# Optimization experiments

Measured on AMD Instinct MI355X. Metric: run time of the kernel, lower is better.

The kernel has to match this reference:

```python
import jax, jax.numpy as jnp
import numpy as np

B, S, I, H = 256, 50, 1024, 512
SENT, DOC = 512, 1024
SEGMENTS, MAXPOS = 4, 25
POS_SZ, SEG_SZ = 50, 50


def _gru_dir(xg, W_hh, b_hh):
    # xg: [S,B,3H] precomputed input gates; returns hidden states [S,B,H]
    Hh = W_hh.shape[1]

    def step(h, xg_t):
        hg = h @ W_hh.T + b_hh  # [B,3H]
        r = jax.nn.sigmoid(xg_t[:, :Hh] + hg[:, :Hh])
        z = jax.nn.sigmoid(xg_t[:, Hh:2 * Hh] + hg[:, Hh:2 * Hh])
        n = jnp.tanh(xg_t[:, 2 * Hh:] + r * hg[:, 2 * Hh:])
        h = (1.0 - z) * n + z * h
        return h, h

    h0 = jnp.zeros((xg.shape[1], Hh), xg.dtype)
    _, hs = jax.lax.scan(step, h0, xg)
    return hs


def setup_inputs() -> dict:
    key = jax.random.key(0)
    ks = jax.random.split(key, 24)
    sc = 0.05
    inp = {
        'x': jax.random.normal(ks[0], (B, S, I), jnp.float32),
        'num_sentences': jnp.full((B,), S, jnp.int32),
        # GRU forward direction
        'W_ih_f': jax.random.normal(ks[1], (3 * H, I), jnp.float32) * sc,
        'W_hh_f': jax.random.normal(ks[2], (3 * H, H), jnp.float32) * sc,
        'b_ih_f': jax.random.normal(ks[3], (3 * H,), jnp.float32) * sc,
        'b_hh_f': jax.random.normal(ks[4], (3 * H,), jnp.float32) * sc,
        # GRU backward direction
        'W_ih_b': jax.random.normal(ks[5], (3 * H, I), jnp.float32) * sc,
        'W_hh_b': jax.random.normal(ks[6], (3 * H, H), jnp.float32) * sc,
        'b_ih_b': jax.random.normal(ks[7], (3 * H,), jnp.float32) * sc,
        'b_hh_b': jax.random.normal(ks[8], (3 * H,), jnp.float32) * sc,
        # sentence_rep: Linear(2H -> SENT) + ReLU
        'W_sent': jax.random.normal(ks[9], (SENT, 2 * H), jnp.float32) * sc,
        'b_sent': jax.random.normal(ks[10], (SENT,), jnp.float32) * sc,
        # content_logits: Linear(SENT -> 1)
        'w_content': jax.random.normal(ks[11], (SENT,), jnp.float32) * sc,
        'b_content': jax.random.normal(ks[12], (1,), jnp.float32) * sc,
        # document_rep: Linear(SENT->DOC), tanh, Linear(DOC->SENT)
        'W_d1': jax.random.normal(ks[13], (DOC, SENT), jnp.float32) * sc,
        'b_d1': jax.random.normal(ks[14], (DOC,), jnp.float32) * sc,
        'W_d2': jax.random.normal(ks[15], (SENT, DOC), jnp.float32) * sc,
        'b_d2': jax.random.normal(ks[16], (SENT,), jnp.float32) * sc,
        # Bilinear(SENT, SENT, 1, bias=False) weight
        'W_sim': jax.random.normal(ks[17], (SENT, SENT), jnp.float32) * sc,
        'bias': jnp.zeros((1,), jnp.float32),
        # position / segment encoders (embedding row 0 is padding -> zeros)
        'pos_emb': (jax.random.normal(ks[18], (MAXPOS + 1, POS_SZ), jnp.float32) * sc).at[0].set(0.0),
        'pos_lin': jax.random.normal(ks[19], (POS_SZ,), jnp.float32) * sc,
        'seg_emb': (jax.random.normal(ks[20], (SEGMENTS + 1, SEG_SZ), jnp.float32) * sc).at[0].set(0.0),
        'seg_lin': jax.random.normal(ks[21], (SEG_SZ,), jnp.float32) * sc,
    }
    return inp


def reference(x, num_sentences, W_ih_f, W_hh_f, b_ih_f, b_hh_f,
              W_ih_b, W_hh_b, b_ih_b, b_hh_b,
              W_sent, b_sent, w_content, b_content,
              W_d1, b_d1, W_d2, b_d2, W_sim, bias,
              pos_emb, pos_lin, seg_emb, seg_lin):
    xs = jnp.transpose(x, (1, 0, 2))  # [S,B,I] (time-major, uniform lengths)

    # Bidirectional GRU
    xg_f = jnp.einsum('sbi,gi->sbg', xs, W_ih_f) + b_ih_f
    hs_f = _gru_dir(xg_f, W_hh_f, b_hh_f)  # [S,B,H]
    xg_b = jnp.einsum('sbi,gi->sbg', xs[::-1], W_ih_b) + b_ih_b
    hs_b = _gru_dir(xg_b, W_hh_b, b_hh_b)[::-1]  # [S,B,H]
    rnn_out = jnp.concatenate([hs_f, hs_b], axis=-1)  # [S,B,2H]
    rnn_out = jnp.transpose(rnn_out, (1, 0, 2))  # [B,S,2H]

    # sentence representations
    sent = jax.nn.relu(jnp.einsum('bsh,dh->bsd', rnn_out, W_sent) + b_sent)  # [B,S,SENT]

    content = jnp.einsum('bsd,d->bs', sent, w_content) + b_content[0]

    avg = sent.sum(axis=1) / num_sentences[:, None].astype(sent.dtype)  # [B,SENT]
    doc = jnp.tanh(avg @ W_d1.T + b_d1) @ W_d2.T + b_d2  # [B,SENT]
    salience = jnp.einsum('bsd,bd->bs', sent, doc)

    # position / segment logits (faithful to original ordering: rel computed pre-clamp)
    abs_pos = jnp.arange(1, S + 1)[None, :].astype(jnp.float32)  # [1,S]
    chunk = jnp.round(num_sentences.astype(jnp.float32) / SEGMENTS)[:, None]  # [B,1]
    rel = jnp.clip(jnp.ceil(abs_pos / chunk), 0, SEGMENTS).astype(jnp.int32)  # [B,S]
    abs_idx = jnp.clip(jnp.arange(1, S + 1), 0, MAXPOS)  # [S]
    pos_logits = pos_emb[abs_idx] @ pos_lin  # [S]
    seg_logits = seg_emb[rel] @ seg_lin  # [B,S]

    static = content + salience + pos_logits[None, :] + seg_logits + bias[0]  # [B,S]

    # sequential novelty scan
    def step(summary, inputs):
        s_t, static_t = inputs  # [B,SENT], [B]
        sim = jnp.einsum('bi,ij,bj->b', s_t, W_sim, jnp.tanh(summary))
        logit = static_t - sim
        summary = summary + s_t * jax.nn.sigmoid(logit)[:, None]
        return summary, logit

    sent_tm = jnp.transpose(sent, (1, 0, 2))  # [S,B,SENT]
    summary0 = jnp.zeros((x.shape[0], SENT), sent.dtype)
    _, logits = jax.lax.scan(step, summary0, (sent_tm, static.T))  # [S,B]
    return logits[:, :, None]  # [S,B,1]
```

## Files before the change

kernel.cpp:

```cpp
#include <hip/hip_runtime.h>
#include <hip/hip_bf16.h>
#include <math.h>

#define B_    256
#define S_    50
#define I_    1024
#define H_    512
#define G3_   1536
#define SENT_ 512
#define DOC_  1024

typedef short bf16x8 __attribute__((ext_vector_type(8)));
typedef float f32x4 __attribute__((ext_vector_type(4)));

__device__ __forceinline__ float sigf(float x) { return 1.0f / (1.0f + __expf(-x)); }

__device__ __forceinline__ void gload16(const void* g, void* l) {
  __builtin_amdgcn_global_load_lds((const __attribute__((address_space(1))) void*)g,
                                   (__attribute__((address_space(3))) void*)l, 16, 0, 0);
}

__global__ __launch_bounds__(256) void mfma_xg(
    const __hip_bfloat16* __restrict__ x,
    const __hip_bfloat16* __restrict__ Wf, const float* __restrict__ bf_,
    const __hip_bfloat16* __restrict__ Wb, const float* __restrict__ bb_,
    __hip_bfloat16* __restrict__ xgf, __hip_bfloat16* __restrict__ xgb) {
  __shared__ __align__(16) short As[128 * 64];
  __shared__ __align__(16) short Ws[128 * 64];
  const int dir = blockIdx.z;
  const __hip_bfloat16* W = dir ? Wb : Wf;
  const float* bias = dir ? bb_ : bf_;
  __hip_bfloat16* out = dir ? xgb : xgf;
  const int tid = threadIdx.x;
  const int m0 = blockIdx.y * 128, n0 = blockIdx.x * 128;
  const int s = blockIdx.y >> 1, b_base = (blockIdx.y & 1) * 128;
  const int s_eff = dir ? (S_ - 1 - s) : s;
  const int lane = tid & 63, w = tid >> 6;
  const int moff = (w & 1) * 64, noff = (w >> 1) * 64;
  const int frow = lane & 15, quad = lane >> 4;
  const int rr = tid >> 3, gs = tid & 7;
  f32x4 acc[4][4] = {};
  for (int kc = 0; kc < I_; kc += 64) {
#pragma unroll
    for (int iss = 0; iss < 4; iss++) {
      int r = iss * 32 + rr;
      int col = kc + ((gs ^ (r & 7)) << 3);
      gload16(x + ((size_t)(b_base + r) * S_ + s_eff) * I_ + col, &As[(iss * 256 + w * 64) * 8]);
    }
#pragma unroll
    for (int iss = 0; iss < 4; iss++) {
      int r = iss * 32 + rr;
      int col = kc + ((gs ^ (r & 7)) << 3);
      gload16(W + (size_t)(n0 + r) * I_ + col, &Ws[(iss * 256 + w * 64) * 8]);
    }
    __syncthreads();
#pragma unroll
    for (int ks = 0; ks < 2; ks++) {
      int kg = ks * 4 + quad;
      bf16x8 af[4], bfr[4];
#pragma unroll
      for (int mf = 0; mf < 4; mf++) {
        int r = moff + mf * 16 + frow;
        af[mf] = *(const bf16x8*)&As[(r * 8 + (kg ^ (r & 7))) * 8];
      }
#pragma unroll
      for (int nf = 0; nf < 4; nf++) {
        int r = noff + nf * 16 + frow;
        bfr[nf] = *(const bf16x8*)&Ws[(r * 8 + (kg ^ (r & 7))) * 8];
      }
#pragma unroll
      for (int mf = 0; mf < 4; mf++)
#pragma unroll
        for (int nf = 0; nf < 4; nf++)
          acc[mf][nf] = __builtin_amdgcn_mfma_f32_16x16x32_bf16(af[mf], bfr[nf], acc[mf][nf], 0, 0, 0);
    }
    __syncthreads();
  }
#pragma unroll
  for (int mf = 0; mf < 4; mf++) {
    int rowb = m0 + moff + mf * 16 + quad * 4;
#pragma unroll
    for (int nf = 0; nf < 4; nf++) {
      int col = n0 + noff + nf * 16 + frow;
      float bv = bias[col];
      f32x4 c = acc[mf][nf];
#pragma unroll
      for (int rg = 0; rg < 4; rg++)
        out[(size_t)(rowb + rg) * G3_ + col] = __float2bfloat16(c[rg] + bv);
    }
  }
}

template <int ACT, bool HASBIAS>
__global__ __launch_bounds__(256) void mfma_nt(
    const __hip_bfloat16* __restrict__ A, const __hip_bfloat16* __restrict__ W,
    const float* __restrict__ bias, __hip_bfloat16* __restrict__ outb, int N, int K) {
  __shared__ __align__(16) short As[128 * 64];
  __shared__ __align__(16) short Ws[128 * 64];
  const int tid = threadIdx.x;
  const int m0 = blockIdx.y * 128, n0 = blockIdx.x * 128;
  const int lane = tid & 63, w = tid >> 6;
  const int moff = (w & 1) * 64, noff = (w >> 1) * 64;
  const int frow = lane & 15, quad = lane >> 4;
  const int rr = tid >> 3, gs = tid & 7;
  f32x4 acc[4][4] = {};
  for (int kc = 0; kc < K; kc += 64) {
#pragma unroll
    for (int iss = 0; iss < 4; iss++) {
      int r = iss * 32 + rr;
      int col = kc + ((gs ^ (r & 7)) << 3);
      gload16(A + (size_t)(m0 + r) * K + col, &As[(iss * 256 + w * 64) * 8]);
    }
#pragma unroll
    for (int iss = 0; iss < 4; iss++) {
      int r = iss * 32 + rr;
      int col = kc + ((gs ^ (r & 7)) << 3);
      gload16(W + (size_t)(n0 + r) * K + col, &Ws[(iss * 256 + w * 64) * 8]);
    }
    __syncthreads();
#pragma unroll
    for (int ks = 0; ks < 2; ks++) {
      int kg = ks * 4 + quad;
      bf16x8 af[4], bfr[4];
#pragma unroll
      for (int mf = 0; mf < 4; mf++) {
        int r = moff + mf * 16 + frow;
        af[mf] = *(const bf16x8*)&As[(r * 8 + (kg ^ (r & 7))) * 8];
      }
#pragma unroll
      for (int nf = 0; nf < 4; nf++) {
        int r = noff + nf * 16 + frow;
        bfr[nf] = *(const bf16x8*)&Ws[(r * 8 + (kg ^ (r & 7))) * 8];
      }
#pragma unroll
      for (int mf = 0; mf < 4; mf++)
#pragma unroll
        for (int nf = 0; nf < 4; nf++)
          acc[mf][nf] = __builtin_amdgcn_mfma_f32_16x16x32_bf16(af[mf], bfr[nf], acc[mf][nf], 0, 0, 0);
    }
    __syncthreads();
  }
#pragma unroll
  for (int mf = 0; mf < 4; mf++) {
    int rowb = m0 + moff + mf * 16 + quad * 4;
#pragma unroll
    for (int nf = 0; nf < 4; nf++) {
      int col = n0 + noff + nf * 16 + frow;
      float bv = HASBIAS ? bias[col] : 0.f;
      f32x4 c = acc[mf][nf];
#pragma unroll
      for (int rg = 0; rg < 4; rg++) {
        float v = c[rg] + bv;
        if (ACT == 1) v = fmaxf(v, 0.f);
        outb[(size_t)(rowb + rg) * N + col] = __float2bfloat16(v);
      }
    }
  }
}

__global__ __launch_bounds__(256, 1) void gru_persistent(
    const __hip_bfloat16* __restrict__ xgf, const __hip_bfloat16* __restrict__ xgb,
    const __hip_bfloat16* __restrict__ Wpf, const __hip_bfloat16* __restrict__ Wpb,
    const float* __restrict__ bhhf, const float* __restrict__ bhhb,
    __hip_bfloat16* __restrict__ h16a, __hip_bfloat16* __restrict__ h16b,
    __hip_bfloat16* __restrict__ rnn,
    unsigned int* __restrict__ arrive) {
  __shared__ __align__(16) short Hs[32 * 512];
  const int bid = blockIdx.x;
  const int dir = bid >> 7;
  const int bt = (bid >> 4) & 7;
  const int jt = bid & 15;
  const int gi = bid >> 4;
  const int tid = threadIdx.x;
  const int w = tid >> 6, lane = tid & 63;
  const int frow = lane & 15, quad = lane >> 4;
  const int wm = w & 1, wn = w >> 1;
  const __hip_bfloat16* xg = dir ? xgb : xgf;
  const __hip_bfloat16* Wp = dir ? Wpb : Wpf;
  const float* bhh = dir ? bhhb : bhhf;

  unsigned int* my_flag = arrive + (size_t)bid * 64;

  const int j = jt * 32 + wn * 16 + frow;
  const int brow0 = bt * 32 + wm * 16 + quad * 4;
  const int ar = wm * 16 + frow;
  const float br = bhh[j], bz = bhh[H_ + j], bn = bhh[2 * H_ + j];

  bf16x8 wf[3][16];
#pragma unroll
  for (int g = 0; g < 3; g++)
#pragma unroll
    for (int ks = 0; ks < 16; ks++)
      wf[g][ks] = *(const bf16x8*)(Wp + (size_t)((jt * 2 + wn) * 48 + g * 16 + frow) * H_ +
                                   ks * 32 + quad * 8);

  float hreg[4] = {0.f, 0.f, 0.f, 0.f};
  union U16 { unsigned long long q[2]; bf16x8 v; };

  for (int t = 0; t < S_; t++) {
    const __hip_bfloat16* hp = (t & 1) ? h16b : h16a;
    __hip_bfloat16* hn = (t & 1) ? h16a : h16b;
    float xgv[4][3];
#pragma unroll
    for (int rg = 0; rg < 4; rg++) {
      const __hip_bfloat16* xr = xg + ((size_t)t * B_ + brow0 + rg) * G3_;
      xgv[rg][0] = __bfloat162float(xr[j]);
      xgv[rg][1] = __bfloat162float(xr[H_ + j]);
      xgv[rg][2] = __bfloat162float(xr[2 * H_ + j]);
    }
    const __hip_bfloat16* hbase = hp + (size_t)(dir * B_ + bt * 32) * H_;
#pragma unroll
    for (int i = 0; i < 8; i++) {
      int c = i * 256 + tid;
      int r = c >> 6, kg = c & 63;
      const unsigned long long* p = (const unsigned long long*)(hbase + (size_t)r * H_ + kg * 8);
      U16 u;
      u.q[0] = __hip_atomic_load(p, __ATOMIC_RELAXED, __HIP_MEMORY_SCOPE_AGENT);
      u.q[1] = __hip_atomic_load(p + 1, __ATOMIC_RELAXED, __HIP_MEMORY_SCOPE_AGENT);
      int q = r * 64 + (kg & 56) + ((kg & 7) ^ (r & 7));
      *(bf16x8*)&Hs[q * 8] = u.v;
    }
    __syncthreads();
    bf16x8 af[16];
#pragma unroll
    for (int ks = 0; ks < 16; ks++) {
      int g2 = ks * 4 + quad;
      int q = ar * 64 + (g2 & 56) + ((g2 & 7) ^ (ar & 7));
      af[ks] = *(const bf16x8*)&Hs[q * 8];
    }
    f32x4 acc[3] = {};
#pragma unroll
    for (int ks = 0; ks < 16; ks++)
#pragma unroll
      for (int g = 0; g < 3; g++)
        acc[g] = __builtin_amdgcn_mfma_f32_16x16x32_bf16(af[ks], wf[g][ks], acc[g], 0, 0, 0);

    const int s_orig = dir ? (S_ - 1 - t) : t;
#pragma unroll
    for (int rg = 0; rg < 4; rg++) {
      int b = brow0 + rg;
      float r = sigf(xgv[rg][0] + acc[0][rg] + br);
      float z = sigf(xgv[rg][1] + acc[1][rg] + bz);
      float n = tanhf(xgv[rg][2] + r * (acc[2][rg] + bn));
      float h = (1.f - z) * n + z * hreg[rg];
      hreg[rg] = h;
      __hip_bfloat16 hb = __float2bfloat16(h);
      unsigned short us;
      __builtin_memcpy(&us, &hb, 2);
      __hip_atomic_store((unsigned short*)(hn + (size_t)(dir * B_ + b) * H_ + j), us,
                         __ATOMIC_RELAXED, __HIP_MEMORY_SCOPE_AGENT);
      rnn[((size_t)b * S_ + s_orig) * (2 * H_) + dir * H_ + j] = hb;
    }

    if (t + 1 < S_) {
      __syncthreads();
      if (tid == 0)
        __hip_atomic_store(my_flag, (unsigned)(t + 1), __ATOMIC_RELAXED,
                           __HIP_MEMORY_SCOPE_AGENT);
      if (w == 0) {
        unsigned int* fl = arrive + (size_t)(gi * 16 + (lane & 15)) * 64;
        for (int spin = 0; spin < (1 << 17); spin++) {
          unsigned v = (lane < 16)
                           ? __hip_atomic_load(fl, __ATOMIC_RELAXED, __HIP_MEMORY_SCOPE_AGENT)
                           : (unsigned)(t + 1);
          if (__ballot(v >= (unsigned)(t + 1)) == ~0ull) break;
          __builtin_amdgcn_s_sleep(1);
        }
      }
      __syncthreads();
    }
  }
}

template <int ACT>
__global__ __launch_bounds__(256) void gemm_nt(const float* __restrict__ A,
                                               const float* __restrict__ W,
                                               const float* __restrict__ bias,
                                               float* __restrict__ C, int N, int K) {
  __shared__ float As[16][68];
  __shared__ float Bs[16][68];
  const int t = threadIdx.x;
  const int tx = t & 15, ty = t >> 4;
  const int m0 = blockIdx.y * 64, n0 = blockIdx.x * 64;
  const int lr = t >> 2, lc = t & 3;
  const float* Arow = A + (size_t)(m0 + lr) * K;
  const float* Wrow = W + (size_t)(n0 + lr) * K;
  float acc[4][4] = {};
  for (int kc = 0; kc < K; kc += 16) {
    float4 av = *(const float4*)(Arow + kc + lc * 4);
    float4 wv = *(const float4*)(Wrow + kc + lc * 4);
    As[lc * 4 + 0][lr] = av.x; As[lc * 4 + 1][lr] = av.y;
    As[lc * 4 + 2][lr] = av.z; As[lc * 4 + 3][lr] = av.w;
    Bs[lc * 4 + 0][lr] = wv.x; Bs[lc * 4 + 1][lr] = wv.y;
    Bs[lc * 4 + 2][lr] = wv.z; Bs[lc * 4 + 3][lr] = wv.w;
    __syncthreads();
#pragma unroll
    for (int k = 0; k < 16; k++) {
      float4 a4 = *(const float4*)&As[k][ty * 4];
      float4 b4 = *(const float4*)&Bs[k][tx * 4];
      float ar[4] = {a4.x, a4.y, a4.z, a4.w};
      float br[4] = {b4.x, b4.y, b4.z, b4.w};
#pragma unroll
      for (int i = 0; i < 4; i++)
#pragma unroll
        for (int jx = 0; jx < 4; jx++) acc[i][jx] = fmaf(ar[i], br[jx], acc[i][jx]);
    }
    __syncthreads();
  }
  float4 bv = *(const float4*)&bias[n0 + tx * 4];
  float bb[4] = {bv.x, bv.y, bv.z, bv.w};
#pragma unroll
  for (int i = 0; i < 4; i++) {
    float o[4];
#pragma unroll
    for (int jx = 0; jx < 4; jx++) {
      float v = acc[i][jx] + bb[jx];
      if (ACT == 1) v = fmaxf(v, 0.f);
      if (ACT == 2) v = tanhf(v);
      o[jx] = v;
    }
    *(float4*)&C[(size_t)(m0 + ty * 4 + i) * N + n0 + tx * 4] = float4{o[0], o[1], o[2], o[3]};
  }
}

#define PREP_CAST1   1536
#define PREP_CAST2   3072
#define PREP_CAST3   3584
#define PREP_PACK1   4352
#define PREP_PACK2   5120
#define PREP_TSIM    6144
#define PREP_ZH      6272
#define PREP_ZF      6288
#define PREP_POS     6289
__global__ __launch_bounds__(256) void prep_all(
    const float* __restrict__ Wihf, const float* __restrict__ Wihb,
    const float* __restrict__ Wsent, const float* __restrict__ Whhf,
    const float* __restrict__ Whhb, const float* __restrict__ Wsim,
    const float* __restrict__ pos_emb, const float* __restrict__ pos_lin,
    const float* __restrict__ seg_emb, const float* __restrict__ seg_lin,
    __hip_bfloat16* __restrict__ Wihf_b, __hip_bfloat16* __restrict__ Wihb_b,
    __hip_bfloat16* __restrict__ Wsent_b, __hip_bfloat16* __restrict__ Wpf,
    __hip_bfloat16* __restrict__ Wpb, __hip_bfloat16* __restrict__ WsimT_b,
    __hip_bfloat16* __restrict__ h16a, unsigned int* __restrict__ arrive,
    float* __restrict__ pos_logits, float* __restrict__ seg_vals) {
  const int blk = blockIdx.x, tid = threadIdx.x;
  if (blk < PREP_CAST2) {
    const float* src = (blk < PREP_CAST1) ? Wihf : Wihb;
    __hip_bfloat16* dst = (blk < PREP_CAST1) ? Wihf_b : Wihb_b;
    int lb = (blk < PREP_CAST1) ? blk : blk - PREP_CAST1;
    int i = lb * 1024 + tid * 4;
    float4 v = *(const float4*)(src + i);
    dst[i] = __float2bfloat16(v.x); dst[i + 1] = __float2bfloat16(v.y);
    dst[i + 2] = __float2bfloat16(v.z); dst[i + 3] = __float2bfloat16(v.w);
  } else if (blk < PREP_CAST3) {
    int i = (blk - PREP_CAST2) * 1024 + tid * 4;
    float4 v = *(const float4*)(Wsent + i);
    Wsent_b[i] = __float2bfloat16(v.x); Wsent_b[i + 1] = __float2bfloat16(v.y);
    Wsent_b[i + 2] = __float2bfloat16(v.z); Wsent_b[i + 3] = __float2bfloat16(v.w);
  } else if (blk < PREP_PACK2) {
    const float* src = (blk < PREP_PACK1) ? Whhf : Whhb;
    __hip_bfloat16* dst = (blk < PREP_PACK1) ? Wpf : Wpb;
    int lb = (blk < PREP_PACK1) ? blk - PREP_CAST3 : blk - PREP_PACK1;
    int e = lb * 1024 + tid * 4;
    int row = e >> 9, k = e & 511;
    int g = row >> 9, j = row & 511;
    int p = (j >> 4) * 48 + g * 16 + (j & 15);
    float4 v = *(const float4*)(src + (size_t)row * 512 + k);
    __hip_bfloat16* d = dst + (size_t)p * 512 + k;
    d[0] = __float2bfloat16(v.x); d[1] = __float2bfloat16(v.y);
    d[2] = __float2bfloat16(v.z); d[3] = __float2bfloat16(v.w);
  } else if (blk < PREP_TSIM) {
    int idx = (blk - PREP_PACK2) * 256 + tid;
    int i = idx >> 9, j = idx & 511;
    WsimT_b[(size_t)j * 512 + i] = __float2bfloat16(Wsim[idx]);
  } else if (blk < PREP_ZH) {
    int i = (blk - PREP_TSIM) * 2048 + tid * 8;
    float4 z = {0.f, 0.f, 0.f, 0.f};
    *(float4*)((short*)h16a + i) = z;
  } else if (blk < PREP_ZF) {
    int i = (blk - PREP_ZH) * 1024 + tid * 4;
    float4 z = {0.f, 0.f, 0.f, 0.f};
    *(float4*)(arrive + i) = z;
  } else {
    if (tid < S_) {
      int idx = tid + 1; if (idx > 25) idx = 25;
      float a = 0.f;
      for (int k = 0; k < 50; k++) a += pos_emb[idx * 50 + k] * pos_lin[k];
      pos_logits[tid] = a;
    }
    if (tid < 5) {
      float a = 0.f;
      for (int k = 0; k < 50; k++) a += seg_emb[tid * 50 + k] * seg_lin[k];
      seg_vals[tid] = a;
    }
  }
}

__global__ void cast_kernel(const float* __restrict__ in, __hip_bfloat16* __restrict__ out, int n) {
  int i = (blockIdx.x * blockDim.x + threadIdx.x) * 4;
  if (i + 3 < n) {
    float4 v = *(const float4*)(in + i);
    out[i + 0] = __float2bfloat16(v.x);
    out[i + 1] = __float2bfloat16(v.y);
    out[i + 2] = __float2bfloat16(v.z);
    out[i + 3] = __float2bfloat16(v.w);
  }
}

__global__ __launch_bounds__(256) void avg_kernel(const __hip_bfloat16* __restrict__ sent,
                                                  const int* __restrict__ ns,
                                                  float* __restrict__ avg) {
  int b = blockIdx.x, tid = threadIdx.x;
  const __hip_bfloat16* base = sent + (size_t)b * S_ * SENT_;
  float a0 = 0.f, a1 = 0.f;
  for (int s = 0; s < S_; s++) {
    a0 += __bfloat162float(base[s * SENT_ + tid]);
    a1 += __bfloat162float(base[s * SENT_ + 256 + tid]);
  }
  float inv = 1.0f / (float)ns[b];
  avg[(size_t)b * SENT_ + tid] = a0 * inv;
  avg[(size_t)b * SENT_ + 256 + tid] = a1 * inv;
}

__global__ __launch_bounds__(64) void static_kernel(
    const __hip_bfloat16* __restrict__ sent, const float* __restrict__ doc,
    const float* __restrict__ wcont, const float* __restrict__ bcont,
    const int* __restrict__ ns, const float* __restrict__ pos_logits,
    const float* __restrict__ seg_vals, const float* __restrict__ bias,
    float* __restrict__ st) {
  int bs = blockIdx.x;
  int b = bs / S_, s = bs % S_;
  int lane = threadIdx.x;
  const __hip_bfloat16* sr = sent + (size_t)bs * SENT_;
  const float* dr = doc + (size_t)b * SENT_;
  float a0 = 0.f, a1 = 0.f;
#pragma unroll
  for (int ii = 0; ii < 8; ii++) {
    int k = ii * 64 + lane;
    float v = __bfloat162float(sr[k]);
    a0 += v * wcont[k];
    a1 += v * dr[k];
  }
#pragma unroll
  for (int off = 32; off; off >>= 1) {
    a0 += __shfl_down(a0, off);
    a1 += __shfl_down(a1, off);
  }
  if (lane == 0) {
    float chunk = rintf((float)ns[b] * 0.25f);
    float relf = ceilf((float)(s + 1) / chunk);
    relf = fminf(fmaxf(relf, 0.f), 4.f);
    int rel = (int)relf;
    st[s * B_ + b] = a0 + bcont[0] + a1 + pos_logits[s] + seg_vals[rel] + bias[0];
  }
}

__global__ __launch_bounds__(256) void novelty_all(
    const __hip_bfloat16* __restrict__ sent, const __hip_bfloat16* __restrict__ U,
    const float* __restrict__ st, float* __restrict__ out) {
  __shared__ float wred[4];
  int b = blockIdx.x, tid = threadIdx.x;
  float s0 = 0.f, s1 = 0.f;
  for (int t = 0; t < S_; t++) {
    const __hip_bfloat16* ur = U + ((size_t)b * S_ + t) * SENT_;
    float p = __bfloat162float(ur[tid]) * tanhf(s0) +
              __bfloat162float(ur[tid + 256]) * tanhf(s1);
#pragma unroll
    for (int off = 32; off; off >>= 1) p += __shfl_down(p, off);
    if ((tid & 63) == 0) wred[tid >> 6] = p;
    __syncthreads();
    float sim = wred[0] + wred[1] + wred[2] + wred[3];
    float logit = st[t * B_ + b] - sim;
    if (tid == 0) out[(size_t)t * B_ + b] = logit;
    float sg = sigf(logit);
    const __hip_bfloat16* sr = sent + ((size_t)b * S_ + t) * SENT_;
    s0 += __bfloat162float(sr[tid]) * sg;
    s1 += __bfloat162float(sr[tid + 256]) * sg;
    __syncthreads();
  }
}

extern "C" void kernel_launch(void* const* d_in, const int* in_sizes, int n_in,
                              void* d_out, int out_size, void* d_ws, size_t ws_size,
                              hipStream_t stream) {
  const float* x = (const float*)d_in[0];
  const int* ns = (const int*)d_in[1];
  const float* Wihf = (const float*)d_in[2];
  const float* Whhf = (const float*)d_in[3];
  const float* bihf = (const float*)d_in[4];
  const float* bhhf = (const float*)d_in[5];
  const float* Wihb = (const float*)d_in[6];
  const float* Whhb = (const float*)d_in[7];
  const float* bihb = (const float*)d_in[8];
  const float* bhhb = (const float*)d_in[9];
  const float* Wsent = (const float*)d_in[10];
  const float* bsent = (const float*)d_in[11];
  const float* wcont = (const float*)d_in[12];
  const float* bcont = (const float*)d_in[13];
  const float* Wd1 = (const float*)d_in[14];
  const float* bd1 = (const float*)d_in[15];
  const float* Wd2 = (const float*)d_in[16];
  const float* bd2 = (const float*)d_in[17];
  const float* Wsim = (const float*)d_in[18];
  const float* bias = (const float*)d_in[19];
  const float* pos_emb = (const float*)d_in[20];
  const float* pos_lin = (const float*)d_in[21];
  const float* seg_emb = (const float*)d_in[22];
  const float* seg_lin = (const float*)d_in[23];
  float* out = (float*)d_out;

  char* base = (char*)d_ws;
  size_t off = 0;
  auto alloc = [&](size_t bytes) { char* p = base + off; off += (bytes + 255) & ~255ull; return p; };
  __hip_bfloat16* xgf_b  = (__hip_bfloat16*)alloc((size_t)S_ * B_ * G3_ * 2);
  __hip_bfloat16* xgb_b  = (__hip_bfloat16*)alloc((size_t)S_ * B_ * G3_ * 2);
  char* region1          = alloc((size_t)B_ * S_ * I_ * 2);
  __hip_bfloat16* x_bf   = (__hip_bfloat16*)region1;
  __hip_bfloat16* sent_b = (__hip_bfloat16*)region1;
  __hip_bfloat16* U_b    = (__hip_bfloat16*)(region1 + (size_t)B_ * S_ * SENT_ * 2);
  __hip_bfloat16* rnn_b  = (__hip_bfloat16*)alloc((size_t)B_ * S_ * 2 * H_ * 2);
  __hip_bfloat16* Wihf_b = (__hip_bfloat16*)alloc((size_t)G3_ * I_ * 2);
  __hip_bfloat16* Wihb_b = (__hip_bfloat16*)alloc((size_t)G3_ * I_ * 2);
  __hip_bfloat16* Wpf    = (__hip_bfloat16*)alloc((size_t)G3_ * H_ * 2);
  __hip_bfloat16* Wpb    = (__hip_bfloat16*)alloc((size_t)G3_ * H_ * 2);
  __hip_bfloat16* Wsent_b= (__hip_bfloat16*)alloc((size_t)SENT_ * 2 * H_ * 2);
  __hip_bfloat16* WsimT_b= (__hip_bfloat16*)alloc((size_t)SENT_ * SENT_ * 2);
  __hip_bfloat16* h16a   = (__hip_bfloat16*)alloc(2 * (size_t)B_ * H_ * 2);
  __hip_bfloat16* h16b   = (__hip_bfloat16*)alloc(2 * (size_t)B_ * H_ * 2);
  unsigned int* arrive   = (unsigned int*)alloc(256 * 64 * 4);
  float* avg             = (float*)alloc((size_t)B_ * SENT_ * 4);
  float* d1buf           = (float*)alloc((size_t)B_ * DOC_ * 4);
  float* doc             = (float*)alloc((size_t)B_ * SENT_ * 4);
  float* st              = (float*)alloc((size_t)S_ * B_ * 4);
  float* poslog          = (float*)alloc(256);
  float* segvals         = (float*)alloc(64);
  (void)ws_size;

  prep_all<<<PREP_POS + 1, 256, 0, stream>>>(
      Wihf, Wihb, Wsent, Whhf, Whhb, Wsim, pos_emb, pos_lin, seg_emb, seg_lin,
      Wihf_b, Wihb_b, Wsent_b, Wpf, Wpb, WsimT_b, h16a, arrive, poslog, segvals);
  cast_kernel<<<(B_ * S_ * I_ / 4 + 255) / 256, 256, 0, stream>>>(x, x_bf, B_ * S_ * I_);

  mfma_xg<<<dim3(G3_ / 128, (S_ * B_) / 128, 2), 256, 0, stream>>>(x_bf, Wihf_b, bihf, Wihb_b, bihb, xgf_b, xgb_b);

  gru_persistent<<<dim3(256), dim3(256), 0, stream>>>(
      xgf_b, xgb_b, Wpf, Wpb, bhhf, bhhb, h16a, h16b, rnn_b, arrive);

  mfma_nt<1, true><<<dim3(SENT_ / 128, (B_ * S_) / 128), 256, 0, stream>>>(rnn_b, Wsent_b, bsent, sent_b, SENT_, 2 * H_);
  avg_kernel<<<B_, 256, 0, stream>>>(sent_b, ns, avg);
  gemm_nt<2><<<dim3(DOC_ / 64, B_ / 64), 256, 0, stream>>>(avg, Wd1, bd1, d1buf, DOC_, SENT_);
  gemm_nt<0><<<dim3(SENT_ / 64, B_ / 64), 256, 0, stream>>>(d1buf, Wd2, bd2, doc, SENT_, DOC_);
  static_kernel<<<B_ * S_, 64, 0, stream>>>(sent_b, doc, wcont, bcont, ns, poslog, segvals, bias, st);

  mfma_nt<0, false><<<dim3(SENT_ / 128, (B_ * S_) / 128), 256, 0, stream>>>(sent_b, WsimT_b, nullptr, U_b, SENT_, SENT_);

  novelty_all<<<B_, 256, 0, stream>>>(sent_b, U_b, st, out);
}
```

Baseline: 695.5 us.

## Fuse x cast into prep, prefetch GRU gates, and shrink novelty/static kernels

Folds the x fp32-to-bf16 cast into the prep kernel to drop one launch. Prefetches the next timestep's input gates before the GRU inter-block barrier so the load latency overlaps the wait. Tiles the Wsim transpose through shared memory for coalesced access, packs four static-logit rows per 256-thread block, and replaces the 256-thread novelty scan with a single-wavefront version using vectorised loads and no block barriers. The costs are more register pressure in the persistent GRU kernel and less parallelism per batch row in the novelty scan.

```diff
diff --git a/kernel.cpp b/kernel.cpp
--- a/kernel.cpp
+++ b/kernel.cpp
@@ -14,6 +14,12 @@
 typedef float f32x4 __attribute__((ext_vector_type(4)));
 
 __device__ __forceinline__ float sigf(float x) { return 1.0f / (1.0f + __expf(-x)); }
+__device__ __forceinline__ float b2f(short s) {
+  unsigned u = ((unsigned)(unsigned short)s) << 16;
+  float f;
+  __builtin_memcpy(&f, &u, 4);
+  return f;
+}
 
 __device__ __forceinline__ void gload16(const void* g, void* l) {
   __builtin_amdgcn_global_load_lds((const __attribute__((address_space(1))) void*)g,
@@ -197,17 +203,18 @@
   float hreg[4] = {0.f, 0.f, 0.f, 0.f};
   union U16 { unsigned long long q[2]; bf16x8 v; };
 
+  float xgv[4][3];
+#pragma unroll
+  for (int rg = 0; rg < 4; rg++) {
+    const __hip_bfloat16* xr = xg + ((size_t)(brow0 + rg)) * G3_;
+    xgv[rg][0] = __bfloat162float(xr[j]);
+    xgv[rg][1] = __bfloat162float(xr[H_ + j]);
+    xgv[rg][2] = __bfloat162float(xr[2 * H_ + j]);
+  }
+
   for (int t = 0; t < S_; t++) {
     const __hip_bfloat16* hp = (t & 1) ? h16b : h16a;
     __hip_bfloat16* hn = (t & 1) ? h16a : h16b;
-    float xgv[4][3];
-#pragma unroll
-    for (int rg = 0; rg < 4; rg++) {
-      const __hip_bfloat16* xr = xg + ((size_t)t * B_ + brow0 + rg) * G3_;
-      xgv[rg][0] = __bfloat162float(xr[j]);
-      xgv[rg][1] = __bfloat162float(xr[H_ + j]);
-      xgv[rg][2] = __bfloat162float(xr[2 * H_ + j]);
-    }
     const __hip_bfloat16* hbase = hp + (size_t)(dir * B_ + bt * 32) * H_;
 #pragma unroll
     for (int i = 0; i < 8; i++) {
@@ -253,6 +260,14 @@
     }
 
     if (t + 1 < S_) {
+      float xgn[4][3];
+#pragma unroll
+      for (int rg = 0; rg < 4; rg++) {
+        const __hip_bfloat16* xr = xg + ((size_t)(t + 1) * B_ + brow0 + rg) * G3_;
+        xgn[rg][0] = __bfloat162float(xr[j]);
+        xgn[rg][1] = __bfloat162float(xr[H_ + j]);
+        xgn[rg][2] = __bfloat162float(xr[2 * H_ + j]);
+      }
       __syncthreads();
       if (tid == 0)
         __hip_atomic_store(my_flag, (unsigned)(t + 1), __ATOMIC_RELAXED,
@@ -268,6 +283,10 @@
         }
       }
       __syncthreads();
+#pragma unroll
+      for (int rg = 0; rg < 4; rg++) {
+        xgv[rg][0] = xgn[rg][0]; xgv[rg][1] = xgn[rg][1]; xgv[rg][2] = xgn[rg][2];
+      }
     }
   }
 }
@@ -323,31 +342,39 @@
   }
 }
 
-#define PREP_CAST1   1536
-#define PREP_CAST2   3072
-#define PREP_CAST3   3584
-#define PREP_PACK1   4352
-#define PREP_PACK2   5120
-#define PREP_TSIM    6144
-#define PREP_ZH      6272
-#define PREP_ZF      6288
-#define PREP_POS     6289
+#define PREP_XC    12800
+#define PREP_CAST1 (PREP_XC + 1536)
+#define PREP_CAST2 (PREP_CAST1 + 1536)
+#define PREP_CAST3 (PREP_CAST2 + 512)
+#define PREP_PACK1 (PREP_CAST3 + 768)
+#define PREP_PACK2 (PREP_PACK1 + 768)
+#define PREP_TSIM  (PREP_PACK2 + 256)
+#define PREP_ZH    (PREP_TSIM + 128)
+#define PREP_ZF    (PREP_ZH + 16)
+#define PREP_POS   (PREP_ZF)
 __global__ __launch_bounds__(256) void prep_all(
-    const float* __restrict__ Wihf, const float* __restrict__ Wihb,
-    const float* __restrict__ Wsent, const float* __restrict__ Whhf,
-    const float* __restrict__ Whhb, const float* __restrict__ Wsim,
+    const float* __restrict__ x, const float* __restrict__ Wihf,
+    const float* __restrict__ Wihb, const float* __restrict__ Wsent,
+    const float* __restrict__ Whhf, const float* __restrict__ Whhb,
+    const float* __restrict__ Wsim,
     const float* __restrict__ pos_emb, const float* __restrict__ pos_lin,
     const float* __restrict__ seg_emb, const float* __restrict__ seg_lin,
+    __hip_bfloat16* __restrict__ x_bf,
     __hip_bfloat16* __restrict__ Wihf_b, __hip_bfloat16* __restrict__ Wihb_b,
     __hip_bfloat16* __restrict__ Wsent_b, __hip_bfloat16* __restrict__ Wpf,
     __hip_bfloat16* __restrict__ Wpb, __hip_bfloat16* __restrict__ WsimT_b,
     __hip_bfloat16* __restrict__ h16a, unsigned int* __restrict__ arrive,
     float* __restrict__ pos_logits, float* __restrict__ seg_vals) {
   const int blk = blockIdx.x, tid = threadIdx.x;
-  if (blk < PREP_CAST2) {
+  if (blk < PREP_XC) {
+    int i = blk * 1024 + tid * 4;
+    float4 v = *(const float4*)(x + i);
+    x_bf[i] = __float2bfloat16(v.x); x_bf[i + 1] = __float2bfloat16(v.y);
+    x_bf[i + 2] = __float2bfloat16(v.z); x_bf[i + 3] = __float2bfloat16(v.w);
+  } else if (blk < PREP_CAST2) {
     const float* src = (blk < PREP_CAST1) ? Wihf : Wihb;
     __hip_bfloat16* dst = (blk < PREP_CAST1) ? Wihf_b : Wihb_b;
-    int lb = (blk < PREP_CAST1) ? blk : blk - PREP_CAST1;
+    int lb = (blk < PREP_CAST1) ? blk - PREP_XC : blk - PREP_CAST1;
     int i = lb * 1024 + tid * 4;
     float4 v = *(const float4*)(src + i);
     dst[i] = __float2bfloat16(v.x); dst[i + 1] = __float2bfloat16(v.y);
@@ -370,9 +397,18 @@
     d[0] = __float2bfloat16(v.x); d[1] = __float2bfloat16(v.y);
     d[2] = __float2bfloat16(v.z); d[3] = __float2bfloat16(v.w);
   } else if (blk < PREP_TSIM) {
-    int idx = (blk - PREP_PACK2) * 256 + tid;
-    int i = idx >> 9, j = idx & 511;
-    WsimT_b[(size_t)j * 512 + i] = __float2bfloat16(Wsim[idx]);
+    __shared__ float tile[32][33];
+    int tb = blk - PREP_PACK2;
+    int ti = tb >> 4, tj = tb & 15;
+    int r = tid >> 3, c4 = (tid & 7) * 4;
+    float4 v = *(const float4*)(Wsim + (size_t)(ti * 32 + r) * 512 + tj * 32 + c4);
+    tile[r][c4] = v.x; tile[r][c4 + 1] = v.y; tile[r][c4 + 2] = v.z; tile[r][c4 + 3] = v.w;
+    __syncthreads();
+    __hip_bfloat16* d = WsimT_b + (size_t)(tj * 32 + r) * 512 + ti * 32 + c4;
+    d[0] = __float2bfloat16(tile[c4][r]);
+    d[1] = __float2bfloat16(tile[c4 + 1][r]);
+    d[2] = __float2bfloat16(tile[c4 + 2][r]);
+    d[3] = __float2bfloat16(tile[c4 + 3][r]);
   } else if (blk < PREP_ZH) {
     int i = (blk - PREP_TSIM) * 2048 + tid * 8;
     float4 z = {0.f, 0.f, 0.f, 0.f};
@@ -396,17 +432,6 @@
   }
 }
 
-__global__ void cast_kernel(const float* __restrict__ in, __hip_bfloat16* __restrict__ out, int n) {
-  int i = (blockIdx.x * blockDim.x + threadIdx.x) * 4;
-  if (i + 3 < n) {
-    float4 v = *(const float4*)(in + i);
-    out[i + 0] = __float2bfloat16(v.x);
-    out[i + 1] = __float2bfloat16(v.y);
-    out[i + 2] = __float2bfloat16(v.z);
-    out[i + 3] = __float2bfloat16(v.w);
-  }
-}
-
 __global__ __launch_bounds__(256) void avg_kernel(const __hip_bfloat16* __restrict__ sent,
                                                   const int* __restrict__ ns,
                                                   float* __restrict__ avg) {
@@ -422,15 +447,15 @@
   avg[(size_t)b * SENT_ + 256 + tid] = a1 * inv;
 }
 
-__global__ __launch_bounds__(64) void static_kernel(
+__global__ __launch_bounds__(256) void static_kernel(
     const __hip_bfloat16* __restrict__ sent, const float* __restrict__ doc,
     const float* __restrict__ wcont, const float* __restrict__ bcont,
     const int* __restrict__ ns, const float* __restrict__ pos_logits,
     const float* __restrict__ seg_vals, const float* __restrict__ bias,
     float* __restrict__ st) {
-  int bs = blockIdx.x;
+  int bs = blockIdx.x * 4 + (threadIdx.x >> 6);
   int b = bs / S_, s = bs % S_;
-  int lane = threadIdx.x;
+  int lane = threadIdx.x & 63;
   const __hip_bfloat16* sr = sent + (size_t)bs * SENT_;
   const float* dr = doc + (size_t)b * SENT_;
   float a0 = 0.f, a1 = 0.f;
@@ -455,28 +480,25 @@
   }
 }
 
-__global__ __launch_bounds__(256) void novelty_all(
+__global__ __launch_bounds__(64) void novelty_wave(
     const __hip_bfloat16* __restrict__ sent, const __hip_bfloat16* __restrict__ U,
     const float* __restrict__ st, float* __restrict__ out) {
-  __shared__ float wred[4];
-  int b = blockIdx.x, tid = threadIdx.x;
-  float s0 = 0.f, s1 = 0.f;
+  int b = blockIdx.x, lane = threadIdx.x;
+  float s[8] = {0.f, 0.f, 0.f, 0.f, 0.f, 0.f, 0.f, 0.f};
   for (int t = 0; t < S_; t++) {
-    const __hip_bfloat16* ur = U + ((size_t)b * S_ + t) * SENT_;
-    float p = __bfloat162float(ur[tid]) * tanhf(s0) +
-              __bfloat162float(ur[tid + 256]) * tanhf(s1);
+    bf16x8 uv = *(const bf16x8*)(U + ((size_t)b * S_ + t) * SENT_ + lane * 8);
+    float p = 0.f;
+#pragma unroll
+    for (int k = 0; k < 8; k++) p += b2f(uv[k]) * tanhf(s[k]);
 #pragma unroll
     for (int off = 32; off; off >>= 1) p += __shfl_down(p, off);
-    if ((tid & 63) == 0) wred[tid >> 6] = p;
-    __syncthreads();
-    float sim = wred[0] + wred[1] + wred[2] + wred[3];
+    float sim = __shfl(p, 0);
     float logit = st[t * B_ + b] - sim;
-    if (tid == 0) out[(size_t)t * B_ + b] = logit;
+    if (lane == 0) out[(size_t)t * B_ + b] = logit;
     float sg = sigf(logit);
-    const __hip_bfloat16* sr = sent + ((size_t)b * S_ + t) * SENT_;
-    s0 += __bfloat162float(sr[tid]) * sg;
-    s1 += __bfloat162float(sr[tid + 256]) * sg;
-    __syncthreads();
+    bf16x8 sv = *(const bf16x8*)(sent + ((size_t)b * S_ + t) * SENT_ + lane * 8);
+#pragma unroll
+    for (int k = 0; k < 8; k++) s[k] += b2f(sv[k]) * sg;
   }
 }
 
@@ -537,9 +559,8 @@
   (void)ws_size;
 
   prep_all<<<PREP_POS + 1, 256, 0, stream>>>(
-      Wihf, Wihb, Wsent, Whhf, Whhb, Wsim, pos_emb, pos_lin, seg_emb, seg_lin,
-      Wihf_b, Wihb_b, Wsent_b, Wpf, Wpb, WsimT_b, h16a, arrive, poslog, segvals);
-  cast_kernel<<<(B_ * S_ * I_ / 4 + 255) / 256, 256, 0, stream>>>(x, x_bf, B_ * S_ * I_);
+      x, Wihf, Wihb, Wsent, Whhf, Whhb, Wsim, pos_emb, pos_lin, seg_emb, seg_lin,
+      x_bf, Wihf_b, Wihb_b, Wsent_b, Wpf, Wpb, WsimT_b, h16a, arrive, poslog, segvals);
 
   mfma_xg<<<dim3(G3_ / 128, (S_ * B_) / 128, 2), 256, 0, stream>>>(x_bf, Wihf_b, bihf, Wihb_b, bihb, xgf_b, xgb_b);
 
@@ -550,9 +571,9 @@
   avg_kernel<<<B_, 256, 0, stream>>>(sent_b, ns, avg);
   gemm_nt<2><<<dim3(DOC_ / 64, B_ / 64), 256, 0, stream>>>(avg, Wd1, bd1, d1buf, DOC_, SENT_);
   gemm_nt<0><<<dim3(SENT_ / 64, B_ / 64), 256, 0, stream>>>(d1buf, Wd2, bd2, doc, SENT_, DOC_);
-  static_kernel<<<B_ * S_, 64, 0, stream>>>(sent_b, doc, wcont, bcont, ns, poslog, segvals, bias, st);
+  static_kernel<<<(B_ * S_) / 4, 256, 0, stream>>>(sent_b, doc, wcont, bcont, ns, poslog, segvals, bias, st);
 
   mfma_nt<0, false><<<dim3(SENT_ / 128, (B_ * S_) / 128), 256, 0, stream>>>(sent_b, WsimT_b, nullptr, U_b, SENT_, SENT_);
 
-  novelty_all<<<B_, 256, 0, stream>>>(sent_b, U_b, st, out);
-}
+  novelty_wave<<<B_, 64, 0, stream>>>(sent_b, U_b, st, out);
+}
```

After: 708.5 us. About the same (+1.9%).
